# Kernel optimization log

Measured on AMD Instinct MI355X. Metric: run time of the kernel, lower is better.

Reference implementation:

```python
import jax, jax.numpy as jnp
import numpy as np

DIM = 384
NUM_HEADS = 12
WS = 8            # window_size
SS = 4            # shift_size
HEAD_DIM = DIM // NUM_HEADS
SCALE = HEAD_DIM ** -0.5
N = WS * WS       # tokens per window
EPS = 1e-5
MLP_HIDDEN = 4 * DIM

# relative position index (static, matches torch buffer construction)
_coords = np.stack(np.meshgrid(np.arange(WS), np.arange(WS), indexing='ij')).reshape(2, -1)
_rel = (_coords[:, :, None] - _coords[:, None, :]).transpose(1, 2, 0)  # [N,N,2]
_rel[..., 0] += WS - 1
_rel[..., 1] += WS - 1
_rel[..., 0] *= 2 * WS - 1
RPI = jnp.asarray(_rel.sum(-1))  # [N,N] int


def layer_norm(x, g, b):
    m = x.mean(-1, keepdims=True)
    v = ((x - m) ** 2).mean(-1, keepdims=True)
    return (x - m) / jnp.sqrt(v + EPS) * g + b


def window_partition(x):
    B, Hh, Ww, C = x.shape
    x = x.reshape(B, Hh // WS, WS, Ww // WS, WS, C).transpose(0, 1, 3, 2, 4, 5)
    return x.reshape(-1, WS, WS, C)


def window_reverse(w, Hh, Ww):
    B = w.shape[0] // ((Hh // WS) * (Ww // WS))
    x = w.reshape(B, Hh // WS, Ww // WS, WS, WS, -1).transpose(0, 1, 3, 2, 4, 5)
    return x.reshape(B, Hh, Ww, -1)


def attention_mask(Hp, Wp):
    # region id along each axis: 0 = [0, Hp-WS), 1 = [Hp-WS, Hp-SS), 2 = [Hp-SS, Hp)
    h_id = np.zeros(Hp, np.int32); h_id[Hp - WS:Hp - SS] = 1; h_id[Hp - SS:] = 2
    w_id = np.zeros(Wp, np.int32); w_id[Wp - WS:Wp - SS] = 1; w_id[Wp - SS:] = 2
    cnt = h_id[:, None] * 3 + w_id[None, :]                      # [Hp, Wp]
    img = jnp.asarray(cnt, jnp.float32).reshape(1, Hp, Wp, 1)
    mw = window_partition(img).reshape(-1, N)                    # [nW, N]
    am = mw[:, None, :] - mw[:, :, None]                         # [nW, N, N]
    return jnp.where(am != 0, jnp.float32(-100.0), jnp.float32(0.0))


def setup_inputs() -> dict:
    key = jax.random.key(0)
    ks = jax.random.split(key, 8)
    B, H, W = 32, 64, 64
    std = 0.02
    return {
        'x': jax.random.normal(ks[0], (B, H * W, DIM), jnp.float32),
        'qkv_w': jax.random.normal(ks[1], (DIM, 3 * DIM), jnp.float32) * std,
        'qkv_b': jnp.zeros((3 * DIM,), jnp.float32),
        'proj_w': jax.random.normal(ks[2], (DIM, DIM), jnp.float32) * std,
        'proj_b': jnp.zeros((DIM,), jnp.float32),
        'rpb_table': jax.random.normal(ks[3], ((2 * WS - 1) * (2 * WS - 1), NUM_HEADS), jnp.float32) * std,
        'n1_g': jnp.ones((DIM,), jnp.float32), 'n1_b': jnp.zeros((DIM,), jnp.float32),
        'n2_g': jnp.ones((DIM,), jnp.float32), 'n2_b': jnp.zeros((DIM,), jnp.float32),
        'fc1_w': jax.random.normal(ks[4], (DIM, MLP_HIDDEN), jnp.float32) * std,
        'fc1_b': jnp.zeros((MLP_HIDDEN,), jnp.float32),
        'fc2_w': jax.random.normal(ks[5], (MLP_HIDDEN, DIM), jnp.float32) * std,
        'fc2_b': jnp.zeros((DIM,), jnp.float32),
        'H': 64, 'W': 64,
    }


def reference(x, qkv_w, qkv_b, proj_w, proj_b, rpb_table, n1_g, n1_b, n2_g, n2_b,
              fc1_w, fc1_b, fc2_w, fc2_b, H, W):
    B, L, C = x.shape
    shortcut = x
    h = layer_norm(x, n1_g, n1_b).reshape(B, H, W, C)
    pad_r = (WS - W % WS) % WS
    pad_b = (WS - H % WS) % WS
    if pad_r or pad_b:
        h = jnp.pad(h, ((0, 0), (0, pad_b), (0, pad_r), (0, 0)))
    Hp, Wp = H + pad_b, W + pad_r
    shifted = jnp.roll(h, shift=(-SS, -SS), axis=(1, 2))
    xw = window_partition(shifted).reshape(-1, N, C)             # [B_, N, C]
    B_ = xw.shape[0]

    qkv = (xw @ qkv_w + qkv_b).reshape(B_, N, 3, NUM_HEADS, HEAD_DIM)
    q = qkv[:, :, 0].transpose(0, 2, 1, 3) * SCALE               # [B_, h, N, d]
    k = qkv[:, :, 1].transpose(0, 2, 1, 3)
    v = qkv[:, :, 2].transpose(0, 2, 1, 3)

    attn = jnp.einsum('bhnd,bhmd->bhnm', q, k)                   # [B_, h, N, N]
    bias = rpb_table[RPI].transpose(2, 0, 1)                     # [h, N, N]
    attn = attn + bias[None]

    mask = attention_mask(Hp, Wp)                                # [nW, N, N]
    nW = mask.shape[0]
    attn = attn.reshape(B_ // nW, nW, NUM_HEADS, N, N) + mask[None, :, None]
    attn = jax.nn.softmax(attn.reshape(B_, NUM_HEADS, N, N), axis=-1)

    out = jnp.einsum('bhnm,bhmd->bhnd', attn, v)
    out = out.transpose(0, 2, 1, 3).reshape(B_, N, C)
    out = out @ proj_w + proj_b

    out = window_reverse(out.reshape(-1, WS, WS, C), Hp, Wp)
    out = jnp.roll(out, shift=(SS, SS), axis=(1, 2))
    out = out[:, :H, :W, :].reshape(B, H * W, C)

    x = shortcut + out
    h2 = layer_norm(x, n2_g, n2_b)
    mlp = jax.nn.gelu(h2 @ fc1_w + fc1_b, approximate=False) @ fc2_w + fc2_b
    return x + mlp
```

## Files before the change

kernel.cpp:

```cpp
#include <hip/hip_runtime.h>
#include <math.h>


#define ROWS_TOTAL 131072
#define NWIN_TOTAL 2048

typedef __attribute__((ext_vector_type(8))) __bf16 bf16x8;
typedef __attribute__((ext_vector_type(4))) float f32x4;
typedef __attribute__((ext_vector_type(8))) unsigned short ushort8;

__device__ __forceinline__ unsigned short f2bf(float f) {
  unsigned u = __builtin_bit_cast(unsigned, f);
  u = (u + 0x7fffu + ((u >> 16) & 1u)) >> 16;
  return (unsigned short)u;
}

__device__ __forceinline__ void gload16(const void* g, void* l) {
  __builtin_amdgcn_global_load_lds(
      (const __attribute__((address_space(1))) unsigned int*)g,
      (__attribute__((address_space(3))) unsigned int*)l, 16, 0, 0);
}

__device__ __forceinline__ int gather_row(int win, int t) {
  int b = win >> 6, wi = (win >> 3) & 7, wj = win & 7;
  int gi = (wi * 8 + (t >> 3) + 4) & 63;
  int gj = (wj * 8 + (t & 7) + 4) & 63;
  return (b << 12) + (gi << 6) + gj;
}

__device__ __forceinline__ void frag_mma(const ushort* As_, const ushort* Bs_,
                                         int wr, int wc, int lane,
                                         f32x4 acc[4][4]) {
  const int go = (((lane >> 4) ^ ((lane >> 1) & 3)) << 3);
  const int lr = lane & 15;
  bf16x8 af[4], bfr[4];
#pragma unroll
  for (int mi = 0; mi < 4; ++mi)
    af[mi] = *(const bf16x8*)(As_ + (wr * 64 + mi * 16 + lr) * 32 + go);
#pragma unroll
  for (int nj = 0; nj < 4; ++nj)
    bfr[nj] = *(const bf16x8*)(Bs_ + (wc * 64 + nj * 16 + lr) * 32 + go);
#pragma unroll
  for (int mi = 0; mi < 4; ++mi)
#pragma unroll
    for (int nj = 0; nj < 4; ++nj)
      acc[mi][nj] = __builtin_amdgcn_mfma_f32_16x16x32_bf16(
          af[mi], bfr[nj], acc[mi][nj], 0, 0, 0);
}

#define VM4() asm volatile("s_waitcnt vmcnt(4)" ::: "memory")
#define VM0() asm volatile("s_waitcnt vmcnt(0)" ::: "memory")
#define SCB() __builtin_amdgcn_sched_barrier(0)
#define BARR() __builtin_amdgcn_s_barrier()

#define STG(B_, T_)                                   \
  { size_t ko = (size_t)(T_) * 64;                    \
    gload16(aS0 + ko, &As[B_][w * 1024]);             \
    gload16(aS1 + ko, &As[B_][w * 1024 + 512]);       \
    gload16(bS0 + ko, &Bs[B_][w * 1024]);             \
    gload16(bS1 + ko, &Bs[B_][w * 1024 + 512]); }

#define GEMM_PIPE(NK)                                               \
  {                                                                 \
    STG(0, 0);                                                      \
    STG(1, 1);                                                      \
    VM4(); SCB(); BARR(); SCB();                                    \
    int cur = 0;                                                    \
    for (int t = 0; t < (NK); ++t) {                                \
      if (t + 2 < (NK)) {                                           \
        int nb = cur + 2; if (nb >= 3) nb -= 3;                     \
        STG(nb, t + 2);                                             \
      }                                                             \
      __builtin_amdgcn_s_setprio(1);                                \
      frag_mma(&As[cur][0], &Bs[cur][0], wr, wc, lane, acc);        \
      __builtin_amdgcn_s_setprio(0);                                \
      if (t + 2 < (NK)) { VM4(); } else { VM0(); }                  \
      SCB(); BARR(); SCB();                                         \
      ++cur; if (cur == 3) cur = 0;                                 \
    }                                                               \
  }

__global__ __launch_bounds__(256) void wprep_k(
    const float* __restrict__ qkvw, const float* __restrict__ projw,
    const float* __restrict__ fc1w, const float* __restrict__ fc2w,
    ushort* __restrict__ wq, ushort* __restrict__ wp,
    ushort* __restrict__ w1, ushort* __restrict__ w2) {
  int gid = blockIdx.x * 256 + threadIdx.x;
  const int S1 = 1152 * 384;
  const int S2 = S1 + 384 * 384;
  const int S3 = S2 + 1536 * 384;
  const int S4 = S3 + 384 * 1536;
  if (gid < S1) {
    int n = gid / 384, k = gid - n * 384;
    wq[gid] = f2bf(qkvw[(size_t)k * 1152 + n]);
  } else if (gid < S2) {
    int i = gid - S1, n = i / 384, k = i - n * 384;
    wp[i] = f2bf(projw[(size_t)k * 384 + n]);
  } else if (gid < S3) {
    int i = gid - S2, n = i / 384, k = i - n * 384;
    w1[i] = f2bf(fc1w[(size_t)k * 1536 + n]);
  } else if (gid < S4) {
    int i = gid - S3, n = i / 1536, k = i - n * 1536;
    w2[i] = f2bf(fc2w[(size_t)k * 384 + n]);
  }
}

__global__ void ln_stats_k(const float* __restrict__ x, float* __restrict__ st) {
  int wid = threadIdx.x >> 6, lane = threadIdx.x & 63;
  int row = (blockIdx.x << 2) + wid;
  const float* p = x + (size_t)row * 384;
  float s = 0.f, ss = 0.f;
#pragma unroll
  for (int c = 0; c < 3; ++c) {
    float2 v = *(const float2*)(p + lane * 2 + c * 128);
    s += v.x + v.y;
    ss += v.x * v.x + v.y * v.y;
  }
#pragma unroll
  for (int o = 32; o > 0; o >>= 1) {
    s += __shfl_down(s, o);
    ss += __shfl_down(ss, o);
  }
  if (lane == 0) {
    float m = s * (1.f / 384.f);
    float var = ss * (1.f / 384.f) - m * m;
    *(float2*)(st + (size_t)row * 2) = make_float2(m, rsqrtf(var + 1e-5f));
  }
}

__global__ __launch_bounds__(256) void ln_apply_k(
    const float* __restrict__ x, const float* __restrict__ st,
    const float* __restrict__ g, const float* __restrict__ b,
    ushort* __restrict__ o) {
  int gid = blockIdx.x * 256 + threadIdx.x;
  int row = gid / 48, c8 = (gid - row * 48) * 8;
  float2 s2 = *(const float2*)(st + (size_t)row * 2);
  const float* xp = x + (size_t)row * 384 + c8;
  float4 v0 = *(const float4*)xp, v1 = *(const float4*)(xp + 4);
  float4 g0 = *(const float4*)(g + c8), g1 = *(const float4*)(g + c8 + 4);
  float4 b0 = *(const float4*)(b + c8), b1 = *(const float4*)(b + c8 + 4);
  float m = s2.x, r = s2.y;
  ushort8 w;
  w[0] = f2bf((v0.x - m) * r * g0.x + b0.x);
  w[1] = f2bf((v0.y - m) * r * g0.y + b0.y);
  w[2] = f2bf((v0.z - m) * r * g0.z + b0.z);
  w[3] = f2bf((v0.w - m) * r * g0.w + b0.w);
  w[4] = f2bf((v1.x - m) * r * g1.x + b1.x);
  w[5] = f2bf((v1.y - m) * r * g1.y + b1.y);
  w[6] = f2bf((v1.z - m) * r * g1.z + b1.z);
  w[7] = f2bf((v1.w - m) * r * g1.w + b1.w);
  *(ushort8*)(o + (size_t)row * 384 + c8) = w;
}

__global__ __launch_bounds__(256) void qkv_mfma_k(
    const ushort* __restrict__ xln, const ushort* __restrict__ wq,
    const float* __restrict__ qkvb, float* __restrict__ qd,
    float* __restrict__ kd, float* __restrict__ vd, int wc0) {
  __shared__ __align__(16) ushort As[3][4096];
  __shared__ __align__(16) ushort Bs[3][4096];
  __shared__ int rowS[128];
  const int tid = threadIdx.x;
  const int w = tid >> 6, lane = tid & 63;
  const int wr = w >> 1, wc = w & 1;
  const int bm = blockIdx.x, n0 = blockIdx.y * 128;
  if (tid < 128) {
    int win = wc0 + bm * 2 + (tid >> 6);
    rowS[tid] = gather_row(win, tid & 63);
  }
  __syncthreads();
  const int rA = w * 32 + (lane >> 2);
  const int sle = (((lane & 3) ^ ((lane >> 3) & 3)) << 4);
  const char* aS0 = (const char*)xln + (size_t)rowS[rA] * 768 + sle;
  const char* aS1 = (const char*)xln + (size_t)rowS[rA + 16] * 768 + sle;
  const char* bS0 = (const char*)wq + (size_t)(n0 + rA) * 768 + sle;
  const char* bS1 = (const char*)wq + (size_t)(n0 + rA + 16) * 768 + sle;
  f32x4 acc[4][4];
#pragma unroll
  for (int i = 0; i < 4; ++i)
#pragma unroll
    for (int j = 0; j < 4; ++j) acc[i][j] = (f32x4)(0.f);
  GEMM_PIPE(12);
  const float scale = 0.17677669529663687f;
#pragma unroll
  for (int mi = 0; mi < 4; ++mi) {
#pragma unroll
    for (int r = 0; r < 4; ++r) {
      int rr = wr * 64 + mi * 16 + ((lane >> 4) << 2) + r;
      int w_rel = bm * 2 + (rr >> 6), t = rr & 63;
#pragma unroll
      for (int nj = 0; nj < 4; ++nj) {
        int nc = n0 + wc * 64 + nj * 16 + (lane & 15);
        float v = acc[mi][nj][r] + qkvb[nc];
        int qi = nc / 384, rem = nc - qi * 384;
        int hh = rem >> 5, d = rem & 31;
        float* base = (qi == 0) ? qd : (qi == 1 ? kd : vd);
        if (qi == 0) v *= scale;
        base[(((size_t)w_rel * 12 + hh) << 11) + (t << 5) + d] = v;
      }
    }
  }
}

__global__ __launch_bounds__(128) void attn_k(
    const float* __restrict__ q, const float* __restrict__ k,
    const float* __restrict__ v, const float* __restrict__ rpb,
    ushort* __restrict__ ao, int wc0) {
  __shared__ __align__(16) float kbuf[2][64][32];
  __shared__ __align__(16) float vbuf[2][64][32];
  __shared__ float bias[2][232];
  __shared__ int region[64];
  const int tid = threadIdx.x;
  const int wid = tid >> 6, lane = tid & 63;
  const int w = blockIdx.x, win = wc0 + w;
  const int head = blockIdx.y * 2 + wid;
  if (tid < 64) {
    int wi = (win >> 3) & 7, wj = win & 7;
    int pi = wi * 8 + (tid >> 3), pj = wj * 8 + (tid & 7);
    int ri = pi < 56 ? 0 : (pi < 60 ? 1 : 2);
    int rj = pj < 56 ? 0 : (pj < 60 ? 1 : 2);
    region[tid] = ri * 3 + rj;
  }
  const size_t hb = ((size_t)w * 12 + head) * 2048;
  const float* kp = k + hb;
  const float* vp = v + hb;
#pragma unroll
  for (int s = 0; s < 8; ++s) {
    int f = s * 64 + lane;
    int r = f >> 3, c = (f & 7) << 2;
    *(float4*)&kbuf[wid][r][c] = *(const float4*)(kp + r * 32 + c);
    *(float4*)&vbuf[wid][r][c] = *(const float4*)(vp + r * 32 + c);
  }
  for (int s = lane; s < 225; s += 64) bias[wid][s] = rpb[s * 12 + head];
  __syncthreads();
  const int i = lane;
  float qr[32];
  const float* qp = q + hb + (i << 5);
#pragma unroll
  for (int c = 0; c < 32; c += 4) {
    float4 t4 = *(const float4*)(qp + c);
    qr[c] = t4.x; qr[c + 1] = t4.y; qr[c + 2] = t4.z; qr[c + 3] = t4.w;
  }
  const int yi = i >> 3, xi = i & 7, regi = region[i];
  float sc[64];
  float mx = -3.0e38f;
#pragma unroll
  for (int j = 0; j < 64; ++j) {
    float a = 0.f;
#pragma unroll
    for (int c = 0; c < 32; c += 4) {
      float4 kv = *(float4*)&kbuf[wid][j][c];
      a = fmaf(qr[c], kv.x, a);
      a = fmaf(qr[c + 1], kv.y, a);
      a = fmaf(qr[c + 2], kv.z, a);
      a = fmaf(qr[c + 3], kv.w, a);
    }
    int dy = yi - (j >> 3) + 7, dx = xi - (j & 7) + 7;
    a += bias[wid][dy * 15 + dx];
    if (region[j] != regi) a -= 100.f;
    sc[j] = a;
    mx = fmaxf(mx, a);
  }
  float sum = 0.f;
#pragma unroll
  for (int j = 0; j < 64; ++j) {
    float e = __expf(sc[j] - mx);
    sc[j] = e;
    sum += e;
  }
  const float inv = 1.f / sum;
  float o[32];
#pragma unroll
  for (int c = 0; c < 32; ++c) o[c] = 0.f;
#pragma unroll
  for (int j = 0; j < 64; ++j) {
    float p = sc[j];
#pragma unroll
    for (int c = 0; c < 32; c += 4) {
      float4 vv = *(float4*)&vbuf[wid][j][c];
      o[c] = fmaf(p, vv.x, o[c]);
      o[c + 1] = fmaf(p, vv.y, o[c + 1]);
      o[c + 2] = fmaf(p, vv.z, o[c + 2]);
      o[c + 3] = fmaf(p, vv.w, o[c + 3]);
    }
  }
  ushort* op = ao + ((size_t)(w * 64 + i)) * 384 + (head << 5);
#pragma unroll
  for (int c = 0; c < 32; c += 8) {
    ushort8 pk;
#pragma unroll
    for (int j2 = 0; j2 < 8; ++j2) pk[j2] = f2bf(o[c + j2] * inv);
    *(ushort8*)(op + c) = pk;
  }
}

__global__ __launch_bounds__(256) void proj_mfma_k(
    const ushort* __restrict__ ao, const ushort* __restrict__ wp,
    const float* __restrict__ pb, const float* __restrict__ x,
    float* __restrict__ x2, int wc0) {
  __shared__ __align__(16) ushort As[3][4096];
  __shared__ __align__(16) ushort Bs[3][4096];
  const int tid = threadIdx.x;
  const int w = tid >> 6, lane = tid & 63;
  const int wr = w >> 1, wc = w & 1;
  const int bm = blockIdx.x, n0 = blockIdx.y * 128;
  const int rA = w * 32 + (lane >> 2);
  const int sle = (((lane & 3) ^ ((lane >> 3) & 3)) << 4);
  const char* aS0 = (const char*)ao + (size_t)(bm * 128 + rA) * 768 + sle;
  const char* aS1 = aS0 + (size_t)16 * 768;
  const char* bS0 = (const char*)wp + (size_t)(n0 + rA) * 768 + sle;
  const char* bS1 = bS0 + (size_t)16 * 768;
  f32x4 acc[4][4];
#pragma unroll
  for (int i = 0; i < 4; ++i)
#pragma unroll
    for (int j = 0; j < 4; ++j) acc[i][j] = (f32x4)(0.f);
  GEMM_PIPE(12);
#pragma unroll
  for (int mi = 0; mi < 4; ++mi) {
#pragma unroll
    for (int r = 0; r < 4; ++r) {
      int rr = wr * 64 + mi * 16 + ((lane >> 4) << 2) + r;
      int lw = (bm * 128 + rr) >> 6, t = rr & 63;
      int gr = gather_row(wc0 + lw, t);
#pragma unroll
      for (int nj = 0; nj < 4; ++nj) {
        int nc = n0 + wc * 64 + nj * 16 + (lane & 15);
        size_t idx = (size_t)gr * 384 + nc;
        x2[idx] = acc[mi][nj][r] + pb[nc] + x[idx];
      }
    }
  }
}

__global__ __launch_bounds__(256) void fc1_mfma_k(
    const ushort* __restrict__ x2ln, const ushort* __restrict__ w1,
    const float* __restrict__ fb, ushort* __restrict__ hm, int row0) {
  __shared__ __align__(16) ushort As[3][4096];
  __shared__ __align__(16) ushort Bs[3][4096];
  const int tid = threadIdx.x;
  const int w = tid >> 6, lane = tid & 63;
  const int wr = w >> 1, wc = w & 1;
  const int bm = blockIdx.x, n0 = blockIdx.y * 128;
  const int rA = w * 32 + (lane >> 2);
  const int sle = (((lane & 3) ^ ((lane >> 3) & 3)) << 4);
  const char* aS0 =
      (const char*)x2ln + (size_t)(row0 + bm * 128 + rA) * 768 + sle;
  const char* aS1 = aS0 + (size_t)16 * 768;
  const char* bS0 = (const char*)w1 + (size_t)(n0 + rA) * 768 + sle;
  const char* bS1 = bS0 + (size_t)16 * 768;
  f32x4 acc[4][4];
#pragma unroll
  for (int i = 0; i < 4; ++i)
#pragma unroll
    for (int j = 0; j < 4; ++j) acc[i][j] = (f32x4)(0.f);
  GEMM_PIPE(12);
#pragma unroll
  for (int mi = 0; mi < 4; ++mi) {
#pragma unroll
    for (int r = 0; r < 4; ++r) {
      int rr = wr * 64 + mi * 16 + ((lane >> 4) << 2) + r;
      size_t lrow = (size_t)(bm * 128 + rr);
#pragma unroll
      for (int nj = 0; nj < 4; ++nj) {
        int nc = n0 + wc * 64 + nj * 16 + (lane & 15);
        float v = acc[mi][nj][r] + fb[nc];
        v = 0.5f * v * (1.f + erff(v * 0.70710678118654752f));
        hm[lrow * 1536 + nc] = f2bf(v);
      }
    }
  }
}

__global__ __launch_bounds__(256) void fc2_mfma_k(
    const ushort* __restrict__ hm, const ushort* __restrict__ w2,
    const float* __restrict__ fb, float* __restrict__ out, int row0) {
  __shared__ __align__(16) ushort As[3][4096];
  __shared__ __align__(16) ushort Bs[3][4096];
  const int tid = threadIdx.x;
  const int w = tid >> 6, lane = tid & 63;
  const int wr = w >> 1, wc = w & 1;
  const int bm = blockIdx.x, n0 = blockIdx.y * 128;
  const int rA = w * 32 + (lane >> 2);
  const int sle = (((lane & 3) ^ ((lane >> 3) & 3)) << 4);
  const char* aS0 = (const char*)hm + (size_t)(bm * 128 + rA) * 3072 + sle;
  const char* aS1 = aS0 + (size_t)16 * 3072;
  const char* bS0 = (const char*)w2 + (size_t)(n0 + rA) * 3072 + sle;
  const char* bS1 = bS0 + (size_t)16 * 3072;
  f32x4 acc[4][4];
#pragma unroll
  for (int i = 0; i < 4; ++i)
#pragma unroll
    for (int j = 0; j < 4; ++j) acc[i][j] = (f32x4)(0.f);
  GEMM_PIPE(48);
#pragma unroll
  for (int mi = 0; mi < 4; ++mi) {
#pragma unroll
    for (int r = 0; r < 4; ++r) {
      int rr = wr * 64 + mi * 16 + ((lane >> 4) << 2) + r;
      size_t grow = (size_t)(row0 + bm * 128 + rr);
#pragma unroll
      for (int nj = 0; nj < 4; ++nj) {
        int nc = n0 + wc * 64 + nj * 16 + (lane & 15);
        size_t idx = grow * 384 + nc;
        out[idx] = out[idx] + acc[mi][nj][r] + fb[nc];
      }
    }
  }
}

extern "C" void kernel_launch(void* const* d_in, const int* in_sizes, int n_in,
                              void* d_out, int out_size, void* d_ws, size_t ws_size,
                              hipStream_t stream) {
  const float* x = (const float*)d_in[0];
  const float* qkv_w = (const float*)d_in[1];
  const float* qkv_b = (const float*)d_in[2];
  const float* proj_w = (const float*)d_in[3];
  const float* proj_b = (const float*)d_in[4];
  const float* rpb = (const float*)d_in[5];
  const float* n1g = (const float*)d_in[6];
  const float* n1b = (const float*)d_in[7];
  const float* n2g = (const float*)d_in[8];
  const float* n2b = (const float*)d_in[9];
  const float* fc1w = (const float*)d_in[10];
  const float* fc1b = (const float*)d_in[11];
  const float* fc2w = (const float*)d_in[12];
  const float* fc2b = (const float*)d_in[13];
  float* out = (float*)d_out;
  char* ws = (char*)d_ws;

  float* st1 = (float*)ws;
  float* st2 = (float*)(ws + 1048576);
  ushort* wq = (ushort*)(ws + 2097152);
  ushort* wp = wq + 442368;
  ushort* w1 = wp + 147456;
  ushort* w2 = w1 + 589824;
  ushort* xln = (ushort*)(ws + 5636096);
  char* scratch = ws + 5636096 + 100663296;
  size_t base = 5636096 + 100663296;
  size_t ssz = (ws_size > base) ? ws_size - base : 0;

  wprep_k<<<6912, 256, 0, stream>>>(qkv_w, proj_w, fc1w, fc2w, wq, wp, w1, w2);
  ln_stats_k<<<ROWS_TOTAL / 4, 256, 0, stream>>>(x, st1);
  ln_apply_k<<<ROWS_TOTAL * 48 / 256, 256, 0, stream>>>(x, st1, n1g, n1b, xln);

  const size_t perwin = 344064;
  int nwc = (int)(ssz / perwin);
  if (nwc > NWIN_TOTAL) nwc = NWIN_TOTAL;
  nwc &= ~1;
  if (nwc < 2) nwc = 2;
  float* qd = (float*)scratch;
  float* kd = qd + (size_t)nwc * 24576;
  float* vd = kd + (size_t)nwc * 24576;
  ushort* ao = (ushort*)(vd + (size_t)nwc * 24576);
  for (int wc0 = 0; wc0 < NWIN_TOTAL; wc0 += nwc) {
    int nw = (NWIN_TOTAL - wc0 < nwc) ? (NWIN_TOTAL - wc0) : nwc;
    qkv_mfma_k<<<dim3(nw / 2, 9), 256, 0, stream>>>(xln, wq, qkv_b, qd, kd, vd, wc0);
    attn_k<<<dim3(nw, 6), 128, 0, stream>>>(qd, kd, vd, rpb, ao, wc0);
    proj_mfma_k<<<dim3(nw / 2, 3), 256, 0, stream>>>(ao, wp, proj_b, x, out, wc0);
  }

  ln_stats_k<<<ROWS_TOTAL / 4, 256, 0, stream>>>(out, st2);
  ln_apply_k<<<ROWS_TOTAL * 48 / 256, 256, 0, stream>>>(out, st2, n2g, n2b, xln);
  const size_t pergrp = 393216;
  int ngc = (int)(ssz / pergrp);
  if (ngc > 1024) ngc = 1024;
  if (ngc < 1) ngc = 1;
  ushort* hm = (ushort*)scratch;
  for (int g0 = 0; g0 < 1024; g0 += ngc) {
    int ng = (1024 - g0 < ngc) ? (1024 - g0) : ngc;
    fc1_mfma_k<<<dim3(ng, 12), 256, 0, stream>>>(xln, w1, fc1b, hm, g0 * 128);
    fc2_mfma_k<<<dim3(ng, 3), 256, 0, stream>>>(hm, w2, fc2b, out, g0 * 128);
  }
}
```

Before: 1.574 ms.

## Deepen GEMM pipeline, fuse layernorm, store QKV in bf16, add XCD-aware block mapping

Several independent changes land together. The GEMM prefetch pipeline grows from 3 to 4 LDS stages. The two-pass layernorm (stats kernel plus apply kernel) becomes a single kernel that keeps the row in registers. Q/K/V intermediates are stored as bf16 instead of fp32, halving their traffic. The grid is transposed and blocks are remapped so that blocks sharing an A tile land on the same XCD for L2 reuse. These changes add LDS pressure, which may lower occupancy, and bf16 QKV adds rounding error to the attention scores.

```diff
diff --git a/kernel.cpp b/kernel.cpp
--- a/kernel.cpp
+++ b/kernel.cpp
@@ -13,6 +13,9 @@
   unsigned u = __builtin_bit_cast(unsigned, f);
   u = (u + 0x7fffu + ((u >> 16) & 1u)) >> 16;
   return (unsigned short)u;
+}
+__device__ __forceinline__ float bf2f(unsigned short u) {
+  return __builtin_bit_cast(float, (unsigned)u << 16);
 }
 
 __device__ __forceinline__ void gload16(const void* g, void* l) {
@@ -48,6 +51,7 @@
           af[mi], bfr[nj], acc[mi][nj], 0, 0, 0);
 }
 
+#define VM8() asm volatile("s_waitcnt vmcnt(8)" ::: "memory")
 #define VM4() asm volatile("s_waitcnt vmcnt(4)" ::: "memory")
 #define VM0() asm volatile("s_waitcnt vmcnt(0)" ::: "memory")
 #define SCB() __builtin_amdgcn_sched_barrier(0)
@@ -64,19 +68,19 @@
   {                                                                 \
     STG(0, 0);                                                      \
     STG(1, 1);                                                      \
-    VM4(); SCB(); BARR(); SCB();                                    \
+    STG(2, 2);                                                      \
+    VM8(); SCB(); BARR(); SCB();                                    \
     int cur = 0;                                                    \
     for (int t = 0; t < (NK); ++t) {                                \
-      if (t + 2 < (NK)) {                                           \
-        int nb = cur + 2; if (nb >= 3) nb -= 3;                     \
-        STG(nb, t + 2);                                             \
-      }                                                             \
+      if (t + 3 < (NK)) STG((cur + 3) & 3, t + 3);                  \
       __builtin_amdgcn_s_setprio(1);                                \
       frag_mma(&As[cur][0], &Bs[cur][0], wr, wc, lane, acc);        \
       __builtin_amdgcn_s_setprio(0);                                \
-      if (t + 2 < (NK)) { VM4(); } else { VM0(); }                  \
+      if (t + 3 < (NK)) { VM8(); }                                  \
+      else if (t + 2 < (NK)) { VM4(); }                             \
+      else { VM0(); }                                               \
       SCB(); BARR(); SCB();                                         \
-      ++cur; if (cur == 3) cur = 0;                                 \
+      cur = (cur + 1) & 3;                                          \
     }                                                               \
   }
 
@@ -105,64 +109,58 @@
   }
 }
 
-__global__ void ln_stats_k(const float* __restrict__ x, float* __restrict__ st) {
+__global__ __launch_bounds__(256) void ln_fused_k(
+    const float* __restrict__ x, const float* __restrict__ g,
+    const float* __restrict__ b, ushort* __restrict__ o) {
   int wid = threadIdx.x >> 6, lane = threadIdx.x & 63;
   int row = (blockIdx.x << 2) + wid;
   const float* p = x + (size_t)row * 384;
+  float2 v[3];
   float s = 0.f, ss = 0.f;
 #pragma unroll
   for (int c = 0; c < 3; ++c) {
-    float2 v = *(const float2*)(p + lane * 2 + c * 128);
-    s += v.x + v.y;
-    ss += v.x * v.x + v.y * v.y;
-  }
-#pragma unroll
-  for (int o = 32; o > 0; o >>= 1) {
-    s += __shfl_down(s, o);
-    ss += __shfl_down(ss, o);
-  }
-  if (lane == 0) {
-    float m = s * (1.f / 384.f);
-    float var = ss * (1.f / 384.f) - m * m;
-    *(float2*)(st + (size_t)row * 2) = make_float2(m, rsqrtf(var + 1e-5f));
-  }
-}
-
-__global__ __launch_bounds__(256) void ln_apply_k(
-    const float* __restrict__ x, const float* __restrict__ st,
-    const float* __restrict__ g, const float* __restrict__ b,
-    ushort* __restrict__ o) {
-  int gid = blockIdx.x * 256 + threadIdx.x;
-  int row = gid / 48, c8 = (gid - row * 48) * 8;
-  float2 s2 = *(const float2*)(st + (size_t)row * 2);
-  const float* xp = x + (size_t)row * 384 + c8;
-  float4 v0 = *(const float4*)xp, v1 = *(const float4*)(xp + 4);
-  float4 g0 = *(const float4*)(g + c8), g1 = *(const float4*)(g + c8 + 4);
-  float4 b0 = *(const float4*)(b + c8), b1 = *(const float4*)(b + c8 + 4);
-  float m = s2.x, r = s2.y;
-  ushort8 w;
-  w[0] = f2bf((v0.x - m) * r * g0.x + b0.x);
-  w[1] = f2bf((v0.y - m) * r * g0.y + b0.y);
-  w[2] = f2bf((v0.z - m) * r * g0.z + b0.z);
-  w[3] = f2bf((v0.w - m) * r * g0.w + b0.w);
-  w[4] = f2bf((v1.x - m) * r * g1.x + b1.x);
-  w[5] = f2bf((v1.y - m) * r * g1.y + b1.y);
-  w[6] = f2bf((v1.z - m) * r * g1.z + b1.z);
-  w[7] = f2bf((v1.w - m) * r * g1.w + b1.w);
-  *(ushort8*)(o + (size_t)row * 384 + c8) = w;
+    v[c] = *(const float2*)(p + lane * 2 + c * 128);
+    s += v[c].x + v[c].y;
+    ss += v[c].x * v[c].x + v[c].y * v[c].y;
+  }
+#pragma unroll
+  for (int off = 1; off < 64; off <<= 1) {
+    s += __shfl_xor(s, off);
+    ss += __shfl_xor(ss, off);
+  }
+  float m = s * (1.f / 384.f);
+  float r = rsqrtf(ss * (1.f / 384.f) - m * m + 1e-5f);
+  ushort* op = o + (size_t)row * 384;
+#pragma unroll
+  for (int c = 0; c < 3; ++c) {
+    float2 gg = *(const float2*)(g + lane * 2 + c * 128);
+    float2 bb = *(const float2*)(b + lane * 2 + c * 128);
+    union { ushort u[2]; unsigned w; } pk;
+    pk.u[0] = f2bf((v[c].x - m) * r * gg.x + bb.x);
+    pk.u[1] = f2bf((v[c].y - m) * r * gg.y + bb.y);
+    *(unsigned*)(op + lane * 2 + c * 128) = pk.w;
+  }
 }
 
 __global__ __launch_bounds__(256) void qkv_mfma_k(
     const ushort* __restrict__ xln, const ushort* __restrict__ wq,
-    const float* __restrict__ qkvb, float* __restrict__ qd,
-    float* __restrict__ kd, float* __restrict__ vd, int wc0) {
-  __shared__ __align__(16) ushort As[3][4096];
-  __shared__ __align__(16) ushort Bs[3][4096];
+    const float* __restrict__ qkvb, ushort* __restrict__ qd,
+    ushort* __restrict__ kd, ushort* __restrict__ vd, int wc0) {
+  __shared__ __align__(16) ushort As[4][4096];
+  __shared__ __align__(16) ushort Bs[4][4096];
   __shared__ int rowS[128];
   const int tid = threadIdx.x;
   const int w = tid >> 6, lane = tid & 63;
   const int wr = w >> 1, wc = w & 1;
-  const int bm = blockIdx.x, n0 = blockIdx.y * 128;
+  int p, bm;
+  {
+    int lin = blockIdx.y * 9 + blockIdx.x;
+    if ((gridDim.y & 7) == 0) {
+      int xcd = lin & 7, q = lin >> 3;
+      p = q % 9; bm = (q / 9) * 8 + xcd;
+    } else { p = blockIdx.x; bm = blockIdx.y; }
+  }
+  const int n0 = p * 128;
   if (tid < 128) {
     int win = wc0 + bm * 2 + (tid >> 6);
     rowS[tid] = gather_row(win, tid & 63);
@@ -193,17 +191,17 @@
         float v = acc[mi][nj][r] + qkvb[nc];
         int qi = nc / 384, rem = nc - qi * 384;
         int hh = rem >> 5, d = rem & 31;
-        float* base = (qi == 0) ? qd : (qi == 1 ? kd : vd);
+        ushort* base = (qi == 0) ? qd : (qi == 1 ? kd : vd);
         if (qi == 0) v *= scale;
-        base[(((size_t)w_rel * 12 + hh) << 11) + (t << 5) + d] = v;
+        base[(((size_t)w_rel * 12 + hh) << 11) + (t << 5) + d] = f2bf(v);
       }
     }
   }
 }
 
 __global__ __launch_bounds__(128) void attn_k(
-    const float* __restrict__ q, const float* __restrict__ k,
-    const float* __restrict__ v, const float* __restrict__ rpb,
+    const ushort* __restrict__ q, const ushort* __restrict__ k,
+    const ushort* __restrict__ v, const float* __restrict__ rpb,
     ushort* __restrict__ ao, int wc0) {
   __shared__ __align__(16) float kbuf[2][64][32];
   __shared__ __align__(16) float vbuf[2][64][32];
@@ -221,24 +219,30 @@
     region[tid] = ri * 3 + rj;
   }
   const size_t hb = ((size_t)w * 12 + head) * 2048;
-  const float* kp = k + hb;
-  const float* vp = v + hb;
-#pragma unroll
-  for (int s = 0; s < 8; ++s) {
+  const ushort* kp = k + hb;
+  const ushort* vp = v + hb;
+#pragma unroll
+  for (int s = 0; s < 4; ++s) {
     int f = s * 64 + lane;
-    int r = f >> 3, c = (f & 7) << 2;
-    *(float4*)&kbuf[wid][r][c] = *(const float4*)(kp + r * 32 + c);
-    *(float4*)&vbuf[wid][r][c] = *(const float4*)(vp + r * 32 + c);
+    int r = f >> 2, c = (f & 3) * 8;
+    ushort8 ku = *(const ushort8*)(kp + r * 32 + c);
+    ushort8 vu = *(const ushort8*)(vp + r * 32 + c);
+#pragma unroll
+    for (int j = 0; j < 8; ++j) {
+      kbuf[wid][r][c + j] = bf2f(ku[j]);
+      vbuf[wid][r][c + j] = bf2f(vu[j]);
+    }
   }
   for (int s = lane; s < 225; s += 64) bias[wid][s] = rpb[s * 12 + head];
   __syncthreads();
   const int i = lane;
   float qr[32];
-  const float* qp = q + hb + (i << 5);
-#pragma unroll
-  for (int c = 0; c < 32; c += 4) {
-    float4 t4 = *(const float4*)(qp + c);
-    qr[c] = t4.x; qr[c + 1] = t4.y; qr[c + 2] = t4.z; qr[c + 3] = t4.w;
+  const ushort* qp = q + hb + (i << 5);
+#pragma unroll
+  for (int c = 0; c < 4; ++c) {
+    ushort8 qu = *(const ushort8*)(qp + c * 8);
+#pragma unroll
+    for (int j = 0; j < 8; ++j) qr[c * 8 + j] = bf2f(qu[j]);
   }
   const int yi = i >> 3, xi = i & 7, regi = region[i];
   float sc[64];
@@ -297,12 +301,20 @@
     const ushort* __restrict__ ao, const ushort* __restrict__ wp,
     const float* __restrict__ pb, const float* __restrict__ x,
     float* __restrict__ x2, int wc0) {
-  __shared__ __align__(16) ushort As[3][4096];
-  __shared__ __align__(16) ushort Bs[3][4096];
+  __shared__ __align__(16) ushort As[4][4096];
+  __shared__ __align__(16) ushort Bs[4][4096];
   const int tid = threadIdx.x;
   const int w = tid >> 6, lane = tid & 63;
   const int wr = w >> 1, wc = w & 1;
-  const int bm = blockIdx.x, n0 = blockIdx.y * 128;
+  int p, bm;
+  {
+    int lin = blockIdx.y * 3 + blockIdx.x;
+    if ((gridDim.y & 7) == 0) {
+      int xcd = lin & 7, q = lin >> 3;
+      p = q % 3; bm = (q / 3) * 8 + xcd;
+    } else { p = blockIdx.x; bm = blockIdx.y; }
+  }
+  const int n0 = p * 128;
   const int rA = w * 32 + (lane >> 2);
   const int sle = (((lane & 3) ^ ((lane >> 3) & 3)) << 4);
   const char* aS0 = (const char*)ao + (size_t)(bm * 128 + rA) * 768 + sle;
@@ -320,8 +332,8 @@
 #pragma unroll
     for (int r = 0; r < 4; ++r) {
       int rr = wr * 64 + mi * 16 + ((lane >> 4) << 2) + r;
-      int lw = (bm * 128 + rr) >> 6, t = rr & 63;
-      int gr = gather_row(wc0 + lw, t);
+      int gl = bm * 128 + rr;
+      int gr = gather_row(wc0 + (gl >> 6), gl & 63);
 #pragma unroll
       for (int nj = 0; nj < 4; ++nj) {
         int nc = n0 + wc * 64 + nj * 16 + (lane & 15);
@@ -335,16 +347,23 @@
 __global__ __launch_bounds__(256) void fc1_mfma_k(
     const ushort* __restrict__ x2ln, const ushort* __restrict__ w1,
     const float* __restrict__ fb, ushort* __restrict__ hm, int row0) {
-  __shared__ __align__(16) ushort As[3][4096];
-  __shared__ __align__(16) ushort Bs[3][4096];
+  __shared__ __align__(16) ushort As[4][4096];
+  __shared__ __align__(16) ushort Bs[4][4096];
   const int tid = threadIdx.x;
   const int w = tid >> 6, lane = tid & 63;
   const int wr = w >> 1, wc = w & 1;
-  const int bm = blockIdx.x, n0 = blockIdx.y * 128;
+  int p, bm;
+  {
+    int lin = blockIdx.y * 12 + blockIdx.x;
+    if ((gridDim.y & 7) == 0) {
+      int xcd = lin & 7, q = lin >> 3;
+      p = q % 12; bm = (q / 12) * 8 + xcd;
+    } else { p = blockIdx.x; bm = blockIdx.y; }
+  }
+  const int n0 = p * 128;
   const int rA = w * 32 + (lane >> 2);
   const int sle = (((lane & 3) ^ ((lane >> 3) & 3)) << 4);
-  const char* aS0 =
-      (const char*)x2ln + (size_t)(row0 + bm * 128 + rA) * 768 + sle;
+  const char* aS0 = (const char*)x2ln + (size_t)(row0 + bm * 128 + rA) * 768 + sle;
   const char* aS1 = aS0 + (size_t)16 * 768;
   const char* bS0 = (const char*)w1 + (size_t)(n0 + rA) * 768 + sle;
   const char* bS1 = bS0 + (size_t)16 * 768;
@@ -374,12 +393,20 @@
 __global__ __launch_bounds__(256) void fc2_mfma_k(
     const ushort* __restrict__ hm, const ushort* __restrict__ w2,
     const float* __restrict__ fb, float* __restrict__ out, int row0) {
-  __shared__ __align__(16) ushort As[3][4096];
-  __shared__ __align__(16) ushort Bs[3][4096];
+  __shared__ __align__(16) ushort As[4][4096];
+  __shared__ __align__(16) ushort Bs[4][4096];
   const int tid = threadIdx.x;
   const int w = tid >> 6, lane = tid & 63;
   const int wr = w >> 1, wc = w & 1;
-  const int bm = blockIdx.x, n0 = blockIdx.y * 128;
+  int p, bm;
+  {
+    int lin = blockIdx.y * 3 + blockIdx.x;
+    if ((gridDim.y & 7) == 0) {
+      int xcd = lin & 7, q = lin >> 3;
+      p = q % 3; bm = (q / 3) * 8 + xcd;
+    } else { p = blockIdx.x; bm = blockIdx.y; }
+  }
+  const int n0 = p * 128;
   const int rA = w * 32 + (lane >> 2);
   const int sle = (((lane & 3) ^ ((lane >> 3) & 3)) << 4);
   const char* aS0 = (const char*)hm + (size_t)(bm * 128 + rA) * 3072 + sle;
@@ -428,47 +455,44 @@
   float* out = (float*)d_out;
   char* ws = (char*)d_ws;
 
-  float* st1 = (float*)ws;
-  float* st2 = (float*)(ws + 1048576);
-  ushort* wq = (ushort*)(ws + 2097152);
+  ushort* wq = (ushort*)ws;
   ushort* wp = wq + 442368;
   ushort* w1 = wp + 147456;
   ushort* w2 = w1 + 589824;
-  ushort* xln = (ushort*)(ws + 5636096);
-  char* scratch = ws + 5636096 + 100663296;
-  size_t base = 5636096 + 100663296;
+  ushort* xln = (ushort*)(ws + 3538944);
+  char* scratch = ws + 3538944 + 100663296;
+  size_t base = 3538944 + 100663296;
   size_t ssz = (ws_size > base) ? ws_size - base : 0;
 
   wprep_k<<<6912, 256, 0, stream>>>(qkv_w, proj_w, fc1w, fc2w, wq, wp, w1, w2);
-  ln_stats_k<<<ROWS_TOTAL / 4, 256, 0, stream>>>(x, st1);
-  ln_apply_k<<<ROWS_TOTAL * 48 / 256, 256, 0, stream>>>(x, st1, n1g, n1b, xln);
-
-  const size_t perwin = 344064;
+  ln_fused_k<<<ROWS_TOTAL / 4, 256, 0, stream>>>(x, n1g, n1b, xln);
+
+  const size_t perwin = 196608;
   int nwc = (int)(ssz / perwin);
   if (nwc > NWIN_TOTAL) nwc = NWIN_TOTAL;
-  nwc &= ~1;
-  if (nwc < 2) nwc = 2;
-  float* qd = (float*)scratch;
-  float* kd = qd + (size_t)nwc * 24576;
-  float* vd = kd + (size_t)nwc * 24576;
-  ushort* ao = (ushort*)(vd + (size_t)nwc * 24576);
+  nwc &= ~15;
+  if (nwc < 16) nwc = 16;
+  ushort* qd = (ushort*)scratch;
+  ushort* kd = qd + (size_t)nwc * 24576;
+  ushort* vd = kd + (size_t)nwc * 24576;
+  ushort* ao = vd + (size_t)nwc * 24576;
   for (int wc0 = 0; wc0 < NWIN_TOTAL; wc0 += nwc) {
     int nw = (NWIN_TOTAL - wc0 < nwc) ? (NWIN_TOTAL - wc0) : nwc;
-    qkv_mfma_k<<<dim3(nw / 2, 9), 256, 0, stream>>>(xln, wq, qkv_b, qd, kd, vd, wc0);
+    qkv_mfma_k<<<dim3(9, nw / 2), 256, 0, stream>>>(xln, wq, qkv_b, qd, kd, vd, wc0);
     attn_k<<<dim3(nw, 6), 128, 0, stream>>>(qd, kd, vd, rpb, ao, wc0);
-    proj_mfma_k<<<dim3(nw / 2, 3), 256, 0, stream>>>(ao, wp, proj_b, x, out, wc0);
-  }
-
-  ln_stats_k<<<ROWS_TOTAL / 4, 256, 0, stream>>>(out, st2);
-  ln_apply_k<<<ROWS_TOTAL * 48 / 256, 256, 0, stream>>>(out, st2, n2g, n2b, xln);
+    proj_mfma_k<<<dim3(3, nw / 2), 256, 0, stream>>>(ao, wp, proj_b, x, out, wc0);
+  }
+
+  ln_fused_k<<<ROWS_TOTAL / 4, 256, 0, stream>>>(out, n2g, n2b, xln);
   const size_t pergrp = 393216;
   int ngc = (int)(ssz / pergrp);
   if (ngc > 1024) ngc = 1024;
-  if (ngc < 1) ngc = 1;
+  ngc &= ~7;
+  if (ngc < 8) ngc = 8;
   ushort* hm = (ushort*)scratch;
   for (int g0 = 0; g0 < 1024; g0 += ngc) {
     int ng = (1024 - g0 < ngc) ? (1024 - g0) : ngc;
-    fc1_mfma_k<<<dim3(ng, 12), 256, 0, stream>>>(xln, w1, fc1b, hm, g0 * 128);
-    fc2_mfma_k<<<dim3(ng, 3), 256, 0, stream>>>(hm, w2, fc2b, out, g0 * 128);
-  }
-}
+    fc1_mfma_k<<<dim3(12, ng), 256, 0, stream>>>(xln, w1, fc1b, hm, g0 * 128);
+    fc2_mfma_k<<<dim3(3, ng), 256, 0, stream>>>(hm, w2, fc2b, out, g0 * 128);
+  }
+}
```

Measured after the change: 1.446 ms. 8.1% less time.
